# Performance work log

Measured on AMD Instinct MI355X. Metric: run time of the kernel, lower is better.

## Reference

```python
import jax, jax.numpy as jnp
import numpy as np

N_NODES = 100000
D = 128
N_EDGES = 500000
EPS = 1e-05


def setup_inputs() -> dict:
    key = jax.random.key(0)
    k1, k2, k3 = jax.random.split(key, 3)
    embed = jax.random.uniform(k1, (N_NODES, D), dtype=jnp.float32)
    weight = jax.random.uniform(k2, (N_EDGES, 1), dtype=jnp.float32)
    edge_idx = jax.random.randint(k3, (N_EDGES, 2), 0, N_NODES, dtype=jnp.int64)
    return {"embed": embed, "weight": weight, "edge_idx": edge_idx}


def reference(embed, weight, edge_idx):
    # Original math: sigmoid(log((A @ B.T) @ w) + 1e-5)
    # where A = embed[edge_idx[:,0]] (E,d), B = embed[edge_idx[:,1]] (E,d), w (E,1).
    # Reassociate (A @ B.T) @ w == A @ (B.T @ w) to avoid the ExE intermediate.
    A = embed[edge_idx[:, 0]]                 # (E, d) gather
    B = embed[edge_idx[:, 1]]                 # (E, d) gather
    btw = jnp.einsum('ed,eo->do', B, weight)  # (d, 1)  tiny contraction
    score = A @ btw                           # (E, 1)
    return jax.nn.sigmoid(jnp.log(score) + EPS)
```

## Files before the change

### kernel.cpp

```cpp
#include <hip/hip_runtime.h>

#define D 128
#define EPS 1e-5f
#define NBLK 2048

__global__ __launch_bounds__(256) void zero_kernel(
    float4* __restrict__ p, int n4)
{
    const int i = blockIdx.x * blockDim.x + threadIdx.x;
    const int stride = gridDim.x * blockDim.x;
    const float4 z = {0.f, 0.f, 0.f, 0.f};
    for (int k = i; k < n4; k += stride) p[k] = z;
}

__global__ __launch_bounds__(256) void wsum_kernel(
    const float* __restrict__ weight,
    const int* __restrict__ eidx,
    float* __restrict__ wsum,
    int nEdges)
{
    const int e = blockIdx.x * blockDim.x + threadIdx.x;
    if (e < nEdges) {
        const int2 p = reinterpret_cast<const int2*>(eidx)[e];
        unsafeAtomicAdd(&wsum[p.y], weight[e]);
    }
}

__global__ __launch_bounds__(256) void btw_partial_kernel(
    const float* __restrict__ embed,
    const float* __restrict__ wsum,
    float* __restrict__ partialT,
    int nNodes)
{
    __shared__ float sbtw[D];
    const int tid = threadIdx.x;
    for (int i = tid; i < D; i += 256) sbtw[i] = 0.f;
    __syncthreads();

    const int j = tid & 31;
    const int hw  = blockIdx.x * 8 + (tid >> 5);
    const int nhw = gridDim.x * 8;

    float4 a0 = {0.f, 0.f, 0.f, 0.f};
    float4 a1 = {0.f, 0.f, 0.f, 0.f};
    int n = hw;
    for (; n + nhw < nNodes; n += 2 * nhw) {
        const float w0 = wsum[n];
        const float w1 = wsum[n + nhw];
        const float4 v0 = reinterpret_cast<const float4*>(embed + (size_t)n * D)[j];
        const float4 v1 = reinterpret_cast<const float4*>(embed + (size_t)(n + nhw) * D)[j];
        a0.x += w0 * v0.x; a0.y += w0 * v0.y; a0.z += w0 * v0.z; a0.w += w0 * v0.w;
        a1.x += w1 * v1.x; a1.y += w1 * v1.y; a1.z += w1 * v1.z; a1.w += w1 * v1.w;
    }
    if (n < nNodes) {
        const float w0 = wsum[n];
        const float4 v0 = reinterpret_cast<const float4*>(embed + (size_t)n * D)[j];
        a0.x += w0 * v0.x; a0.y += w0 * v0.y; a0.z += w0 * v0.z; a0.w += w0 * v0.w;
    }
    a0.x += a1.x; a0.y += a1.y; a0.z += a1.z; a0.w += a1.w;

    atomicAdd(&sbtw[4 * j + 0], a0.x);
    atomicAdd(&sbtw[4 * j + 1], a0.y);
    atomicAdd(&sbtw[4 * j + 2], a0.z);
    atomicAdd(&sbtw[4 * j + 3], a0.w);
    __syncthreads();
    if (tid < D) partialT[(size_t)tid * NBLK + blockIdx.x] = sbtw[tid];
}

__global__ __launch_bounds__(256) void btw_reduce_kernel(
    const float* __restrict__ partialT,
    float* __restrict__ btw)
{
    __shared__ float red[256];
    const int d = blockIdx.x;
    const int tid = threadIdx.x;
    float s = 0.f;
    const float* row = partialT + (size_t)d * NBLK;
    #pragma unroll
    for (int k = tid; k < NBLK; k += 256) s += row[k];
    red[tid] = s;
    __syncthreads();
    for (int off = 128; off > 0; off >>= 1) {
        if (tid < off) red[tid] += red[tid + off];
        __syncthreads();
    }
    if (tid == 0) btw[d] = red[0];
}

__global__ __launch_bounds__(256) void snode_kernel(
    const float* __restrict__ embed,
    const float* __restrict__ btw,
    float* __restrict__ snode,
    int nNodes)
{
    const int tid = threadIdx.x;
    const int j = tid & 31;
    const float4 bt = reinterpret_cast<const float4*>(btw)[j];
    const int hw  = blockIdx.x * 8 + (tid >> 5);
    const int nhw = gridDim.x * 8;

    int n = hw;
    for (; n + nhw < nNodes; n += 2 * nhw) {
        const float4 v0 = reinterpret_cast<const float4*>(embed + (size_t)n * D)[j];
        const float4 v1 = reinterpret_cast<const float4*>(embed + (size_t)(n + nhw) * D)[j];
        float s0 = v0.x * bt.x + v0.y * bt.y + v0.z * bt.z + v0.w * bt.w;
        float s1 = v1.x * bt.x + v1.y * bt.y + v1.z * bt.z + v1.w * bt.w;
        #pragma unroll
        for (int m = 1; m < 32; m <<= 1) {
            s0 += __shfl_xor(s0, m, 64);
            s1 += __shfl_xor(s1, m, 64);
        }
        if (j == 0) {
            snode[n] = s0;
            snode[n + nhw] = s1;
        }
    }
    if (n < nNodes) {
        const float4 v0 = reinterpret_cast<const float4*>(embed + (size_t)n * D)[j];
        float s0 = v0.x * bt.x + v0.y * bt.y + v0.z * bt.z + v0.w * bt.w;
        #pragma unroll
        for (int m = 1; m < 32; m <<= 1)
            s0 += __shfl_xor(s0, m, 64);
        if (j == 0) snode[n] = s0;
    }
}

__global__ __launch_bounds__(256) void out_kernel(
    const int* __restrict__ eidx,
    const float* __restrict__ snode,
    float* __restrict__ out,
    int nEdges)
{
    const int e = blockIdx.x * blockDim.x + threadIdx.x;
    if (e < nEdges) {
        const int2 p = reinterpret_cast<const int2*>(eidx)[e];
        const float x = logf(snode[p.x]) + EPS;
        out[e] = 1.f / (1.f + expf(-x));
    }
}

extern "C" void kernel_launch(void* const* d_in, const int* in_sizes, int n_in,
                              void* d_out, int out_size, void* d_ws, size_t ws_size,
                              hipStream_t stream) {
    const float* embed  = (const float*)d_in[0];
    const float* weight = (const float*)d_in[1];
    const int*   eidx   = (const int*)d_in[2];
    float* out = (float*)d_out;

    const int nEdges = in_sizes[1];
    const int nNodes = in_sizes[0] / D;

    float* wsum     = (float*)d_ws;
    float* btw      = wsum + nNodes;
    float* snode    = btw + D;
    float* partialT = snode + nNodes;

    const int nZero4 = (nNodes + 3) / 4;
    const int eBlocks = (nEdges + 255) / 256;

    zero_kernel       <<<512,     256, 0, stream>>>((float4*)d_ws, nZero4);
    wsum_kernel       <<<eBlocks, 256, 0, stream>>>(weight, eidx, wsum, nEdges);
    btw_partial_kernel<<<NBLK,    256, 0, stream>>>(embed, wsum, partialT, nNodes);
    btw_reduce_kernel <<<D,       256, 0, stream>>>(partialT, btw);
    snode_kernel      <<<NBLK,    256, 0, stream>>>(embed, btw, snode, nNodes);
    out_kernel        <<<eBlocks, 256, 0, stream>>>(eidx, snode, out, nEdges);
}
```

Measured before the change: 71.19 us.

## Vectorize edge kernels, simplify sigmoid-log, and use contiguous row blocks for scans

The wsum and out kernels now each handle two edges per thread, using int4/float2 loads and a paired float2 store. The out kernel replaces log plus sigmoid with the algebraic identity s/(s+c), which removes the transcendental calls. The node scan kernels stop using grid-stride loops and instead give each half-wave 8 contiguous rows loaded up front, which increases memory-level parallelism. The grid size for these scans now depends on the node count, giving about 1563 blocks instead of 2048. The zero kernel is launched one element per thread.

```diff
diff --git a/kernel.cpp b/kernel.cpp
--- a/kernel.cpp
+++ b/kernel.cpp
@@ -2,15 +2,14 @@
 
 #define D 128
 #define EPS 1e-5f
-#define NBLK 2048
+#define SCAN_ROWS 8
+#define HW_PER_BLK 8
 
 __global__ __launch_bounds__(256) void zero_kernel(
     float4* __restrict__ p, int n4)
 {
     const int i = blockIdx.x * blockDim.x + threadIdx.x;
-    const int stride = gridDim.x * blockDim.x;
-    const float4 z = {0.f, 0.f, 0.f, 0.f};
-    for (int k = i; k < n4; k += stride) p[k] = z;
+    if (i < n4) p[i] = {0.f, 0.f, 0.f, 0.f};
 }
 
 __global__ __launch_bounds__(256) void wsum_kernel(
@@ -19,65 +18,77 @@
     float* __restrict__ wsum,
     int nEdges)
 {
-    const int e = blockIdx.x * blockDim.x + threadIdx.x;
-    if (e < nEdges) {
-        const int2 p = reinterpret_cast<const int2*>(eidx)[e];
-        unsafeAtomicAdd(&wsum[p.y], weight[e]);
+    const int t = blockIdx.x * blockDim.x + threadIdx.x;
+    const int e0 = 2 * t;
+    if (e0 + 1 < nEdges) {
+        const int4   p = reinterpret_cast<const int4*>(eidx)[t];
+        const float2 w = reinterpret_cast<const float2*>(weight)[t];
+        unsafeAtomicAdd(&wsum[p.y], w.x);
+        unsafeAtomicAdd(&wsum[p.w], w.y);
+    } else if (e0 < nEdges) {
+        unsafeAtomicAdd(&wsum[eidx[2 * e0 + 1]], weight[e0]);
     }
 }
 
-__global__ __launch_bounds__(256) void btw_partial_kernel(
+__global__ __launch_bounds__(256, 8) void btw_partial_kernel(
     const float* __restrict__ embed,
     const float* __restrict__ wsum,
     float* __restrict__ partialT,
-    int nNodes)
+    int nNodes, int nScanBlk)
 {
     __shared__ float sbtw[D];
     const int tid = threadIdx.x;
     for (int i = tid; i < D; i += 256) sbtw[i] = 0.f;
     __syncthreads();
 
-    const int j = tid & 31;
-    const int hw  = blockIdx.x * 8 + (tid >> 5);
-    const int nhw = gridDim.x * 8;
+    const int j  = tid & 31;
+    const int hw = blockIdx.x * HW_PER_BLK + (tid >> 5);
+    const int n0 = hw * SCAN_ROWS;
 
-    float4 a0 = {0.f, 0.f, 0.f, 0.f};
-    float4 a1 = {0.f, 0.f, 0.f, 0.f};
-    int n = hw;
-    for (; n + nhw < nNodes; n += 2 * nhw) {
-        const float w0 = wsum[n];
-        const float w1 = wsum[n + nhw];
-        const float4 v0 = reinterpret_cast<const float4*>(embed + (size_t)n * D)[j];
-        const float4 v1 = reinterpret_cast<const float4*>(embed + (size_t)(n + nhw) * D)[j];
-        a0.x += w0 * v0.x; a0.y += w0 * v0.y; a0.z += w0 * v0.z; a0.w += w0 * v0.w;
-        a1.x += w1 * v1.x; a1.y += w1 * v1.y; a1.z += w1 * v1.z; a1.w += w1 * v1.w;
+    float4 acc = {0.f, 0.f, 0.f, 0.f};
+    if (n0 + SCAN_ROWS <= nNodes) {
+        float4 v[SCAN_ROWS];
+        float  w[SCAN_ROWS];
+        #pragma unroll
+        for (int r = 0; r < SCAN_ROWS; ++r)
+            v[r] = reinterpret_cast<const float4*>(embed + (size_t)(n0 + r) * D)[j];
+        #pragma unroll
+        for (int r = 0; r < SCAN_ROWS; ++r)
+            w[r] = wsum[n0 + r];
+        #pragma unroll
+        for (int r = 0; r < SCAN_ROWS; ++r) {
+            acc.x += w[r] * v[r].x;
+            acc.y += w[r] * v[r].y;
+            acc.z += w[r] * v[r].z;
+            acc.w += w[r] * v[r].w;
+        }
+    } else {
+        for (int r = 0; r < SCAN_ROWS && n0 + r < nNodes; ++r) {
+            const float  w = wsum[n0 + r];
+            const float4 v = reinterpret_cast<const float4*>(embed + (size_t)(n0 + r) * D)[j];
+            acc.x += w * v.x; acc.y += w * v.y; acc.z += w * v.z; acc.w += w * v.w;
+        }
     }
-    if (n < nNodes) {
-        const float w0 = wsum[n];
-        const float4 v0 = reinterpret_cast<const float4*>(embed + (size_t)n * D)[j];
-        a0.x += w0 * v0.x; a0.y += w0 * v0.y; a0.z += w0 * v0.z; a0.w += w0 * v0.w;
-    }
-    a0.x += a1.x; a0.y += a1.y; a0.z += a1.z; a0.w += a1.w;
 
-    atomicAdd(&sbtw[4 * j + 0], a0.x);
-    atomicAdd(&sbtw[4 * j + 1], a0.y);
-    atomicAdd(&sbtw[4 * j + 2], a0.z);
-    atomicAdd(&sbtw[4 * j + 3], a0.w);
+    atomicAdd(&sbtw[4*j+0], acc.x);
+    atomicAdd(&sbtw[4*j+1], acc.y);
+    atomicAdd(&sbtw[4*j+2], acc.z);
+    atomicAdd(&sbtw[4*j+3], acc.w);
     __syncthreads();
-    if (tid < D) partialT[(size_t)tid * NBLK + blockIdx.x] = sbtw[tid];
+    if (tid < D) partialT[(size_t)tid * nScanBlk + blockIdx.x] = sbtw[tid];
 }
 
 __global__ __launch_bounds__(256) void btw_reduce_kernel(
     const float* __restrict__ partialT,
-    float* __restrict__ btw)
+    float* __restrict__ btw,
+    int nScanBlk)
 {
     __shared__ float red[256];
     const int d = blockIdx.x;
     const int tid = threadIdx.x;
     float s = 0.f;
-    const float* row = partialT + (size_t)d * NBLK;
-    #pragma unroll
-    for (int k = tid; k < NBLK; k += 256) s += row[k];
+    const float* row = partialT + (size_t)d * nScanBlk;
+    for (int k = tid; k < nScanBlk; k += 256) s += row[k];
     red[tid] = s;
     __syncthreads();
     for (int off = 128; off > 0; off >>= 1) {
@@ -87,7 +98,7 @@
     if (tid == 0) btw[d] = red[0];
 }
 
-__global__ __launch_bounds__(256) void snode_kernel(
+__global__ __launch_bounds__(256, 8) void snode_kernel(
     const float* __restrict__ embed,
     const float* __restrict__ btw,
     float* __restrict__ snode,
@@ -96,32 +107,38 @@
     const int tid = threadIdx.x;
     const int j = tid & 31;
     const float4 bt = reinterpret_cast<const float4*>(btw)[j];
-    const int hw  = blockIdx.x * 8 + (tid >> 5);
-    const int nhw = gridDim.x * 8;
+    const int hw = blockIdx.x * HW_PER_BLK + (tid >> 5);
+    const int n0 = hw * SCAN_ROWS;
 
-    int n = hw;
-    for (; n + nhw < nNodes; n += 2 * nhw) {
-        const float4 v0 = reinterpret_cast<const float4*>(embed + (size_t)n * D)[j];
-        const float4 v1 = reinterpret_cast<const float4*>(embed + (size_t)(n + nhw) * D)[j];
-        float s0 = v0.x * bt.x + v0.y * bt.y + v0.z * bt.z + v0.w * bt.w;
-        float s1 = v1.x * bt.x + v1.y * bt.y + v1.z * bt.z + v1.w * bt.w;
+    if (n0 + SCAN_ROWS <= nNodes) {
+        float4 v[SCAN_ROWS];
+        #pragma unroll
+        for (int r = 0; r < SCAN_ROWS; ++r)
+            v[r] = reinterpret_cast<const float4*>(embed + (size_t)(n0 + r) * D)[j];
+        float s[SCAN_ROWS];
+        #pragma unroll
+        for (int r = 0; r < SCAN_ROWS; ++r)
+            s[r] = v[r].x*bt.x + v[r].y*bt.y + v[r].z*bt.z + v[r].w*bt.w;
         #pragma unroll
         for (int m = 1; m < 32; m <<= 1) {
-            s0 += __shfl_xor(s0, m, 64);
-            s1 += __shfl_xor(s1, m, 64);
+            #pragma unroll
+            for (int r = 0; r < SCAN_ROWS; ++r)
+                s[r] += __shfl_xor(s[r], m, 64);
         }
         if (j == 0) {
-            snode[n] = s0;
-            snode[n + nhw] = s1;
+            float4 o0 = {s[0], s[1], s[2], s[3]};
+            float4 o1 = {s[4], s[5], s[6], s[7]};
+            reinterpret_cast<float4*>(snode + n0)[0] = o0;
+            reinterpret_cast<float4*>(snode + n0)[1] = o1;
         }
-    }
-    if (n < nNodes) {
-        const float4 v0 = reinterpret_cast<const float4*>(embed + (size_t)n * D)[j];
-        float s0 = v0.x * bt.x + v0.y * bt.y + v0.z * bt.z + v0.w * bt.w;
-        #pragma unroll
-        for (int m = 1; m < 32; m <<= 1)
-            s0 += __shfl_xor(s0, m, 64);
-        if (j == 0) snode[n] = s0;
+    } else if (n0 < nNodes) {
+        for (int r = 0; r < SCAN_ROWS && n0 + r < nNodes; ++r) {
+            const float4 v = reinterpret_cast<const float4*>(embed + (size_t)(n0 + r) * D)[j];
+            float s = v.x*bt.x + v.y*bt.y + v.z*bt.z + v.w*bt.w;
+            #pragma unroll
+            for (int m = 1; m < 32; m <<= 1) s += __shfl_xor(s, m, 64);
+            if (j == 0) snode[n0 + r] = s;
+        }
     }
 }
 
@@ -131,11 +148,18 @@
     float* __restrict__ out,
     int nEdges)
 {
-    const int e = blockIdx.x * blockDim.x + threadIdx.x;
-    if (e < nEdges) {
-        const int2 p = reinterpret_cast<const int2*>(eidx)[e];
-        const float x = logf(snode[p.x]) + EPS;
-        out[e] = 1.f / (1.f + expf(-x));
+    const float c = 0.9999900000499999f;
+    const int t = blockIdx.x * blockDim.x + threadIdx.x;
+    const int e0 = 2 * t;
+    if (e0 + 1 < nEdges) {
+        const int4 p = reinterpret_cast<const int4*>(eidx)[t];
+        const float sa = snode[p.x];
+        const float sb = snode[p.z];
+        float2 o = { sa / (sa + c), sb / (sb + c) };
+        reinterpret_cast<float2*>(out)[t] = o;
+    } else if (e0 < nEdges) {
+        const float s = snode[eidx[2 * e0]];
+        out[e0] = s / (s + c);
     }
 }
 
@@ -155,13 +179,15 @@
     float* snode    = btw + D;
     float* partialT = snode + nNodes;
 
-    const int nZero4 = (nNodes + 3) / 4;
-    const int eBlocks = (nEdges + 255) / 256;
+    const int nZero4   = (nNodes + 3) / 4;
+    const int zBlocks  = (nZero4 + 255) / 256;
+    const int pBlocks  = ((nEdges + 1) / 2 + 255) / 256;
+    const int nScanBlk = (nNodes + SCAN_ROWS * HW_PER_BLK - 1) / (SCAN_ROWS * HW_PER_BLK);
 
-    zero_kernel       <<<512,     256, 0, stream>>>((float4*)d_ws, nZero4);
-    wsum_kernel       <<<eBlocks, 256, 0, stream>>>(weight, eidx, wsum, nEdges);
-    btw_partial_kernel<<<NBLK,    256, 0, stream>>>(embed, wsum, partialT, nNodes);
-    btw_reduce_kernel <<<D,       256, 0, stream>>>(partialT, btw);
-    snode_kernel      <<<NBLK,    256, 0, stream>>>(embed, btw, snode, nNodes);
-    out_kernel        <<<eBlocks, 256, 0, stream>>>(eidx, snode, out, nEdges);
+    zero_kernel       <<<zBlocks,  256, 0, stream>>>((float4*)d_ws, nZero4);
+    wsum_kernel       <<<pBlocks,  256, 0, stream>>>(weight, eidx, wsum, nEdges);
+    btw_partial_kernel<<<nScanBlk, 256, 0, stream>>>(embed, wsum, partialT, nNodes, nScanBlk);
+    btw_reduce_kernel <<<D,        256, 0, stream>>>(partialT, btw, nScanBlk);
+    snode_kernel      <<<nScanBlk, 256, 0, stream>>>(embed, btw, snode, nNodes);
+    out_kernel        <<<pBlocks,  256, 0, stream>>>(eidx, snode, out, nEdges);
 }
```

Result: faster. 67.54 us (-5.1%).
